# Performance work log

Hardware: AMD Instinct MI355X
Metric: run time of the kernel (lower is better)

The kernel has to match this reference:

```python
import jax, jax.numpy as jnp
import numpy as np

F_DIM = 64
USER_SIZES = [11577, 11, 11, 11, 11, 21, 7]
URL_SIZES = [4733, 21, 7, 11, 11]
USER_OFF = np.concatenate([[0], np.cumsum(USER_SIZES)[:-1]]).astype(np.int64)
URL_OFF = np.concatenate([[0], np.cumsum(URL_SIZES)[:-1]]).astype(np.int64)
EPS = 1e-6


def feature_embed(table, offsets, feats):
    # feats: [..., F] int ids per feature column; sum of per-column embeddings -> [..., F_DIM]
    return jnp.take(table, feats + offsets, axis=0).sum(axis=-2)


def cosine(a, b):
    # cosine similarity along last axis, torch-style eps clamping of each norm
    dot = jnp.sum(a * b, axis=-1)
    na = jnp.maximum(jnp.sqrt(jnp.sum(a * a, axis=-1)), EPS)
    nb = jnp.maximum(jnp.sqrt(jnp.sum(b * b, axis=-1)), EPS)
    return dot / (na * nb)


def graph_attention(f_embed, weight_list, center_embed):
    # f_embed: [..., K, D], weight_list: [..., K], center_embed: [..., D]
    cw = cosine(f_embed, jnp.expand_dims(center_embed, -2))      # [..., K]
    cw = jax.nn.softmax(cw, axis=-1)
    new = jax.nn.relu(f_embed * weight_list[..., None]) * cw[..., None]
    return new.sum(axis=-2)                                      # [..., D]


def linear(x, W, b):
    return x @ W.T + b


def setup_inputs() -> dict:
    key = jax.random.key(0)
    ks = jax.random.split(key, 24)
    N, K = 8192, 8
    ri = lambda k, shp, hi: jax.random.randint(k, shp, 0, hi, dtype=jnp.int64)
    rf = lambda k, shp: jax.random.uniform(k, shp, dtype=jnp.float32)
    rn = lambda k, shp, s: jax.random.normal(k, shp, dtype=jnp.float32) * s
    inp = {
        'url_idxs': ri(ks[0], (N,), 4733),
        'user_f_list': ri(ks[1], (N, 7), 7),
        'url_f_list': ri(ks[2], (N, 5), 7),
        'user_1_user_f_list': ri(ks[3], (N, K, 7), 7),
        'user_1_user_weight': rf(ks[4], (N, K)),
        'user_1_url_f_list': ri(ks[5], (N, K, 5), 7),
        'user_1_url_weight': rf(ks[6], (N, K)),
        'user_2_user_f_list': ri(ks[7], (N, K, K, 7), 7),
        'user_2_user_weight': rf(ks[8], (N, K, K)),
        'user_2_url_f_list': ri(ks[9], (N, K, K, 5), 7),
        'user_2_url_weight': rf(ks[10], (N, K, K)),
        'url_2_user_f_list': ri(ks[11], (N, K, K, 7), 7),
        'url_2_user_weight': rf(ks[12], (N, K, K)),
        'url_2_url_f_list': ri(ks[13], (N, K, K, 5), 7),
        'url_2_url_weight': rf(ks[14], (N, K, K)),
        'user_table': rn(ks[15], (int(sum(USER_SIZES)), F_DIM), 0.1),
        'url_table': rn(ks[16], (int(sum(URL_SIZES)), F_DIM), 0.1),
        'W2': rn(ks[17], (F_DIM, 2 * F_DIM), 0.05), 'b2': jnp.zeros((F_DIM,), jnp.float32),
        'W1': rn(ks[18], (F_DIM, 2 * F_DIM), 0.05), 'b1': jnp.zeros((F_DIM,), jnp.float32),
        'Wo': rn(ks[19], (2, 2 * F_DIM), 0.05), 'bo': jnp.zeros((2,), jnp.float32),
    }
    return inp


def reference(url_idxs, user_f_list, url_f_list,
              user_1_user_f_list, user_1_user_weight,
              user_1_url_f_list, user_1_url_weight,
              user_2_user_f_list, user_2_user_weight,
              user_2_url_f_list, user_2_url_weight,
              url_2_user_f_list, url_2_user_weight,
              url_2_url_f_list, url_2_url_weight,
              user_table, url_table, W2, b2, W1, b1, Wo, bo):
    user_off = jnp.asarray(USER_OFF)
    url_off = jnp.asarray(URL_OFF)

    # --- url branch (hop2 -> hop1) ---
    ori_user_1_url = feature_embed(url_table, url_off, user_1_url_f_list)        # [N,K,D]
    ori_url_2_user = feature_embed(user_table, user_off, url_2_user_f_list)      # [N,K,K,D]
    url_2_user_new = graph_attention(ori_url_2_user, url_2_user_weight, ori_user_1_url)
    ori_url_2_url = feature_embed(url_table, url_off, url_2_url_f_list)
    url_2_url_new = graph_attention(ori_url_2_url, url_2_url_weight, ori_user_1_url)
    user_1_url = (url_2_user_new + url_2_url_new) / 2
    user_1_url = jax.nn.relu(linear(jnp.concatenate([ori_user_1_url, user_1_url], axis=2), W2, b2))

    # --- user branch (hop2 -> hop1) ---
    ori_user_1_user = feature_embed(user_table, user_off, user_1_user_f_list)
    ori_user_2_user = feature_embed(user_table, user_off, user_2_user_f_list)
    user_2_user_new = graph_attention(ori_user_2_user, user_2_user_weight, ori_user_1_user)
    ori_user_2_url = feature_embed(url_table, url_off, user_2_url_f_list)
    user_2_url_new = graph_attention(ori_user_2_url, user_2_url_weight, ori_user_1_user)
    user_1_user = (user_2_user_new + user_2_url_new) / 2
    user_1_user = jax.nn.relu(linear(jnp.concatenate([ori_user_1_user, user_1_user], axis=2), W2, b2))

    # --- hop1 -> center ---
    ori_user = feature_embed(user_table, user_off, user_f_list)                  # [N,D]
    u1_url_new = graph_attention(user_1_url, user_1_url_weight, ori_user)
    u1_user_new = graph_attention(user_1_user, user_1_user_weight, ori_user)
    user_embed = (u1_url_new + u1_user_new) / 2
    user_embed = jax.nn.relu(linear(jnp.concatenate([ori_user, user_embed], axis=1), W1, b1))

    url_embed = feature_embed(url_table, url_off, url_f_list)                    # [N,D]
    out = linear(jnp.concatenate([user_embed, url_embed], axis=1), Wo, bo)       # [N,2]
    return jax.nn.softmax(out, axis=1)
```

## Files before the change

### kernel.cpp

```cpp
#include <hip/hip_runtime.h>

#define TPB 256
#define SPB 4
#define NSAMP 8192
#define EPS 1e-6f

#define O_CENT   0
#define O_CNORM  1088
#define O_ORI    1104
#define O_ONORM  1168
#define O_URLEMB 1172
#define O_JOB    1236
#define O_IDX    3412
#define O_H1     3520
#define O_W      5056
#define O_W1H    5312
#define O_GA1    5328
#define O_PART   5464
#define O_PP     5728
#define DYN_SZ   6800

__device__ __forceinline__ float sx(float v, int m) { return __shfl_xor(v, m, 64); }

__global__ __launch_bounds__(TPB, 3)
void gcn_fused(const int* __restrict__ g_user_f, const int* __restrict__ g_url_f,
               const int* __restrict__ g_u1u_f, const float* __restrict__ g_u1u_w,
               const int* __restrict__ g_u1l_f, const float* __restrict__ g_u1l_w,
               const int* __restrict__ g_u2u_f, const float* __restrict__ g_u2u_w,
               const int* __restrict__ g_u2l_f, const float* __restrict__ g_u2l_w,
               const int* __restrict__ g_l2u_f, const float* __restrict__ g_l2u_w,
               const int* __restrict__ g_l2l_f, const float* __restrict__ g_l2l_w,
               const float* __restrict__ g_utab, const float* __restrict__ g_ltab,
               const float* __restrict__ g_W2, const float* __restrict__ g_b2,
               const float* __restrict__ g_W1, const float* __restrict__ g_b1,
               const float* __restrict__ g_Wo, const float* __restrict__ g_bo,
               float* __restrict__ g_out)
{
  __shared__ __align__(16) float s_lut[5712];
  __shared__ __align__(16) float s_dyn[DYN_SZ];

  const int tid  = threadIdx.x;
  const int wv   = tid >> 6;
  const int lane = tid & 63;
  const int g    = (tid >> 4) & 3;
  const int l    = tid & 15;

  float* s_ulut = s_lut;
  float* s_llut = s_lut + 3332;
  int*   s_idx  = (int*)&s_dyn[O_IDX];
  float* s_h1   = &s_dyn[O_H1];

  #pragma unroll
  for (int c = 0; c < 7; ++c) {
    constexpr int uoff[7] = {0,11577,11588,11599,11610,11621,11642};
    for (int i = tid; i < 7*64; i += TPB) {
      const int id = i >> 6, d = i & 63;
      s_ulut[(c*7+id)*68 + d] = g_utab[(uoff[c]+id)*64 + d];
    }
  }
  #pragma unroll
  for (int c = 0; c < 5; ++c) {
    constexpr int loff[5] = {0,4733,4754,4761,4772};
    for (int i = tid; i < 7*64; i += TPB) {
      const int id = i >> 6, d = i & 63;
      s_llut[(c*7+id)*68 + d] = g_ltab[(loff[c]+id)*64 + d];
    }
  }

  float w2r[32], w1r[32];
  float* s_tmp = s_dyn;
#define LOAD_WT(Wg, wr)                                              \
  for (int half = 0; half < 2; ++half) {                             \
    __syncthreads();                                                 \
    for (int i = tid; i < 4096; i += TPB) {                          \
      const int r = i >> 7, j = i & 127;                             \
      s_tmp[r*132 + j] = Wg[(half*32 + r)*128 + j];                  \
    }                                                                \
    __syncthreads();                                                 \
    if ((lane >> 5) == half) {                                       \
      const int lr = lane & 31;                                      \
      _Pragma("unroll")                                              \
      for (int jj = 0; jj < 32; ++jj)                                \
        wr[jj] = s_tmp[lr*132 + wv*32 + jj];                         \
    }                                                                \
  }
  LOAD_WT(g_W2, w2r)
  LOAD_WT(g_W1, w1r)
#undef LOAD_WT

  const float b2v = g_b2[lane];
  const float b1v = g_b1[lane];

  const int jb = wv;
  const int F3 = (jb == 0 || jb == 2) ? 7 : 5;
  const float* lut3 = (jb == 0 || jb == 2) ? s_ulut : s_llut;
  const int ibase3 = (jb == 0) ? 876 : (jb == 1) ? 1324 : (jb == 2) ? 108 : 556;
  const int b3 = jb >> 1;

  for (int s = 0; s < SPB; ++s) {
    const int n = blockIdx.x * SPB + s;
    __syncthreads();

    for (int i = tid; i < 56;  i += TPB) s_idx[i]        = g_u1u_f[n*56 + i];
    for (int i = tid; i < 40;  i += TPB) s_idx[56 + i]   = g_u1l_f[n*40 + i];
    if (tid < 7) s_idx[96 + tid]  = g_user_f[n*7 + tid];
    if (tid < 5) s_idx[103 + tid] = g_url_f[n*5 + tid];
    for (int i = tid; i < 448; i += TPB) s_idx[108 + i]  = g_u2u_f[n*448 + i];
    for (int i = tid; i < 320; i += TPB) s_idx[556 + i]  = g_u2l_f[n*320 + i];
    for (int i = tid; i < 448; i += TPB) s_idx[876 + i]  = g_l2u_f[n*448 + i];
    for (int i = tid; i < 320; i += TPB) s_idx[1324 + i] = g_l2l_f[n*320 + i];
    for (int i = tid; i < 64; i += TPB) {
      s_dyn[O_W + i]       = g_l2u_w[n*64 + i];
      s_dyn[O_W + 64 + i]  = g_l2l_w[n*64 + i];
      s_dyn[O_W + 128 + i] = g_u2u_w[n*64 + i];
      s_dyn[O_W + 192 + i] = g_u2l_w[n*64 + i];
    }
    if (tid < 8)       s_dyn[O_W1H + tid] = g_u1u_w[n*8 + tid];
    else if (tid < 16) s_dyn[O_W1H + tid] = g_u1l_w[n*8 + (tid - 8)];
    __syncthreads();

    {
      const int gg = tid >> 4;
      const bool isUser = gg >= 8;
      const int k = gg & 7;
      const float* lut = isUser ? s_ulut : s_llut;
      const int F  = isUser ? 7 : 5;
      const int ib = isUser ? (k*7) : (56 + k*5);
      float4 e = make_float4(0.f,0.f,0.f,0.f);
      for (int c = 0; c < F; ++c) {
        const int id = s_idx[ib + c];
        const float4 t = *(const float4*)&lut[(c*7 + id)*68 + l*4];
        e.x += t.x; e.y += t.y; e.z += t.z; e.w += t.w;
      }
      float na2 = e.x*e.x + e.y*e.y + e.z*e.z + e.w*e.w;
      #pragma unroll
      for (int m = 1; m <= 8; m <<= 1) na2 += sx(na2, m);
      const int bsel = isUser ? 1 : 0;
      *(float4*)&s_dyn[O_CENT + bsel*544 + k*68 + l*4] = e;
      if (l == 0) s_dyn[O_CNORM + bsel*8 + k] = fmaxf(sqrtf(na2), EPS);

      if (gg < 2) {
        const float* lutm = (gg == 0) ? s_ulut : s_llut;
        const int Fm  = (gg == 0) ? 7 : 5;
        const int ibm = (gg == 0) ? 96 : 103;
        float4 em = make_float4(0.f,0.f,0.f,0.f);
        for (int c = 0; c < Fm; ++c) {
          const int id = s_idx[ibm + c];
          const float4 t = *(const float4*)&lutm[(c*7 + id)*68 + l*4];
          em.x += t.x; em.y += t.y; em.z += t.z; em.w += t.w;
        }
        if (gg == 0) {
          float nn = em.x*em.x + em.y*em.y + em.z*em.z + em.w*em.w;
          #pragma unroll
          for (int m = 1; m <= 8; m <<= 1) nn += sx(nn, m);
          *(float4*)&s_dyn[O_ORI + l*4] = em;
          if (l == 0) s_dyn[O_ONORM] = fmaxf(sqrtf(nn), EPS);
        } else {
          *(float4*)&s_dyn[O_URLEMB + l*4] = em;
        }
      }
    }
    __syncthreads();

    {
      const float* wb = &s_dyn[O_W + jb*64];
      for (int k1 = 0; k1 < 8; ++k1) {
        const float4 c4 = *(const float4*)&s_dyn[O_CENT + b3*544 + k1*68 + l*4];
        const float nb = s_dyn[O_CNORM + b3*8 + k1];
        float4 ek0, ek1; float cs0, cs1;
        #pragma unroll
        for (int p = 0; p < 2; ++p) {
          const int node = k1*8 + p*4 + g;
          const int* ip = &s_idx[ibase3 + node*F3];
          float4 e = make_float4(0.f,0.f,0.f,0.f);
          for (int c = 0; c < F3; ++c) {
            const float4 t = *(const float4*)&lut3[(c*7 + ip[c])*68 + l*4];
            e.x += t.x; e.y += t.y; e.z += t.z; e.w += t.w;
          }
          float dot = e.x*c4.x + e.y*c4.y + e.z*c4.z + e.w*c4.w;
          float na2 = e.x*e.x + e.y*e.y + e.z*e.z + e.w*e.w;
          #pragma unroll
          for (int m = 1; m <= 8; m <<= 1) { dot += sx(dot, m); na2 += sx(na2, m); }
          const float cs = dot / (fmaxf(sqrtf(na2), EPS) * nb);
          if (p == 0) { ek0 = e; cs0 = cs; } else { ek1 = e; cs1 = cs; }
        }
        float mx = fmaxf(cs0, cs1);
        mx = fmaxf(mx, sx(mx, 16)); mx = fmaxf(mx, sx(mx, 32));
        const float e0 = expf(cs0 - mx), e1 = expf(cs1 - mx);
        float ss = e0 + e1;
        ss += sx(ss, 16); ss += sx(ss, 32);
        const float w0 = wb[k1*8 + g], w1 = wb[k1*8 + 4 + g];
        float ax = fmaxf(ek0.x*w0, 0.f)*e0 + fmaxf(ek1.x*w1, 0.f)*e1;
        float ay = fmaxf(ek0.y*w0, 0.f)*e0 + fmaxf(ek1.y*w1, 0.f)*e1;
        float az = fmaxf(ek0.z*w0, 0.f)*e0 + fmaxf(ek1.z*w1, 0.f)*e1;
        float aw = fmaxf(ek0.w*w0, 0.f)*e0 + fmaxf(ek1.w*w1, 0.f)*e1;
        ax += sx(ax,16); ay += sx(ay,16); az += sx(az,16); aw += sx(aw,16);
        ax += sx(ax,32); ay += sx(ay,32); az += sx(az,32); aw += sx(aw,32);
        const float sc = 0.5f / ss;
        if (g == 0)
          *(float4*)&s_dyn[O_JOB + jb*544 + k1*68 + l*4] =
              make_float4(ax*sc, ay*sc, az*sc, aw*sc);
      }
    }
    __syncthreads();

    for (int i = tid; i < 1088; i += TPB) {
      const int pr = i / 544, rem = i - pr*544;
      const int dst = O_JOB + (pr*2)*544 + rem;
      s_dyn[dst] += s_dyn[dst + 544];
    }
    __syncthreads();

    for (int bt = 0; bt < 4; ++bt) {
      float acc[4];
      #pragma unroll
      for (int r = 0; r < 4; ++r) {
        const int rr = bt*4 + r;
        const int branch = rr >> 3, k = rr & 7;
        const float* xp = (wv < 2)
            ? &s_dyn[O_CENT + branch*544 + k*68 + wv*32]
            : &s_dyn[O_JOB  + (branch*2)*544 + k*68 + (wv - 2)*32];
        float a = 0.f;
        #pragma unroll
        for (int j4 = 0; j4 < 8; ++j4) {
          const float4 xv = *(const float4*)&xp[j4*4];
          a += xv.x * w2r[j4*4 + 0];
          a += xv.y * w2r[j4*4 + 1];
          a += xv.z * w2r[j4*4 + 2];
          a += xv.w * w2r[j4*4 + 3];
        }
        acc[r] = a;
      }
      #pragma unroll
      for (int r = 0; r < 4; ++r)
        s_dyn[O_PP + wv*264 + r*66 + lane] = acc[r];
      __syncthreads();
      {
        const int r = wv, o = lane;
        const int rr = bt*4 + r;
        const int branch = rr >> 3, k = rr & 7;
        float v = b2v;
        #pragma unroll
        for (int q = 0; q < 4; ++q) v += s_dyn[O_PP + q*264 + r*66 + o];
        s_h1[branch*544 + k*68 + o] = fmaxf(v, 0.f);
      }
      __syncthreads();
    }

    if (wv < 2) {
      const float4 c4 = *(const float4*)&s_dyn[O_ORI + l*4];
      const float nb = s_dyn[O_ONORM];
      const float* h1b = &s_h1[wv*544];
      const int wofs = (wv == 0) ? 8 : 0;
      float4 ek0, ek1; float cs0, cs1;
      #pragma unroll
      for (int p = 0; p < 2; ++p) {
        const int k = p*4 + g;
        const float4 e = *(const float4*)&h1b[k*68 + l*4];
        float dot = e.x*c4.x + e.y*c4.y + e.z*c4.z + e.w*c4.w;
        float na2 = e.x*e.x + e.y*e.y + e.z*e.z + e.w*e.w;
        #pragma unroll
        for (int m = 1; m <= 8; m <<= 1) { dot += sx(dot, m); na2 += sx(na2, m); }
        const float cs = dot / (fmaxf(sqrtf(na2), EPS) * nb);
        if (p == 0) { ek0 = e; cs0 = cs; } else { ek1 = e; cs1 = cs; }
      }
      float mx = fmaxf(cs0, cs1);
      mx = fmaxf(mx, sx(mx, 16)); mx = fmaxf(mx, sx(mx, 32));
      const float e0 = expf(cs0 - mx), e1 = expf(cs1 - mx);
      float ss = e0 + e1;
      ss += sx(ss, 16); ss += sx(ss, 32);
      const float w0 = s_dyn[O_W1H + wofs + g], w1 = s_dyn[O_W1H + wofs + 4 + g];
      float ax = fmaxf(ek0.x*w0, 0.f)*e0 + fmaxf(ek1.x*w1, 0.f)*e1;
      float ay = fmaxf(ek0.y*w0, 0.f)*e0 + fmaxf(ek1.y*w1, 0.f)*e1;
      float az = fmaxf(ek0.z*w0, 0.f)*e0 + fmaxf(ek1.z*w1, 0.f)*e1;
      float aw = fmaxf(ek0.w*w0, 0.f)*e0 + fmaxf(ek1.w*w1, 0.f)*e1;
      ax += sx(ax,16); ay += sx(ay,16); az += sx(az,16); aw += sx(aw,16);
      ax += sx(ax,32); ay += sx(ay,32); az += sx(az,32); aw += sx(aw,32);
      const float sc = 0.5f / ss;
      if (g == 0)
        *(float4*)&s_dyn[O_GA1 + wv*68 + l*4] =
            make_float4(ax*sc, ay*sc, az*sc, aw*sc);
    }
    __syncthreads();

    {
      float a = 0.f;
      if (wv < 2) {
        const float* xp = &s_dyn[O_ORI + wv*32];
        #pragma unroll
        for (int j4 = 0; j4 < 8; ++j4) {
          const float4 xv = *(const float4*)&xp[j4*4];
          a += xv.x*w1r[j4*4+0] + xv.y*w1r[j4*4+1] + xv.z*w1r[j4*4+2] + xv.w*w1r[j4*4+3];
        }
      } else {
        const float* xa = &s_dyn[O_GA1 + (wv-2)*32];
        const float* xb = &s_dyn[O_GA1 + 68 + (wv-2)*32];
        #pragma unroll
        for (int j4 = 0; j4 < 8; ++j4) {
          const float4 va = *(const float4*)&xa[j4*4];
          const float4 vb = *(const float4*)&xb[j4*4];
          a += (va.x+vb.x)*w1r[j4*4+0] + (va.y+vb.y)*w1r[j4*4+1]
             + (va.z+vb.z)*w1r[j4*4+2] + (va.w+vb.w)*w1r[j4*4+3];
        }
      }
      s_dyn[O_PART + wv*66 + lane] = a;
    }
    __syncthreads();

    if (wv == 0) {
      float ue = b1v;
      #pragma unroll
      for (int q = 0; q < 4; ++q) ue += s_dyn[O_PART + q*66 + lane];
      ue = fmaxf(ue, 0.f);
      const float ul = s_dyn[O_URLEMB + lane];
      float p0 = ue * g_Wo[lane]       + ul * g_Wo[64 + lane];
      float p1 = ue * g_Wo[128 + lane] + ul * g_Wo[192 + lane];
      #pragma unroll
      for (int m = 1; m <= 32; m <<= 1) { p0 += sx(p0, m); p1 += sx(p1, m); }
      if (lane == 0) {
        const float l0 = p0 + g_bo[0], l1 = p1 + g_bo[1];
        const float mx = fmaxf(l0, l1);
        const float q0 = expf(l0 - mx), q1 = expf(l1 - mx);
        const float rinv = 1.f / (q0 + q1);
        g_out[n*2 + 0] = q0 * rinv;
        g_out[n*2 + 1] = q1 * rinv;
      }
    }
  }
}

extern "C" void kernel_launch(void* const* d_in, const int* in_sizes, int n_in,
                              void* d_out, int out_size, void* d_ws, size_t ws_size,
                              hipStream_t stream) {
  (void)in_sizes; (void)n_in; (void)d_ws; (void)ws_size; (void)out_size;
  const int*   g_user_f = (const int*)d_in[1];
  const int*   g_url_f  = (const int*)d_in[2];
  const int*   g_u1u_f  = (const int*)d_in[3];
  const float* g_u1u_w  = (const float*)d_in[4];
  const int*   g_u1l_f  = (const int*)d_in[5];
  const float* g_u1l_w  = (const float*)d_in[6];
  const int*   g_u2u_f  = (const int*)d_in[7];
  const float* g_u2u_w  = (const float*)d_in[8];
  const int*   g_u2l_f  = (const int*)d_in[9];
  const float* g_u2l_w  = (const float*)d_in[10];
  const int*   g_l2u_f  = (const int*)d_in[11];
  const float* g_l2u_w  = (const float*)d_in[12];
  const int*   g_l2l_f  = (const int*)d_in[13];
  const float* g_l2l_w  = (const float*)d_in[14];
  const float* g_utab   = (const float*)d_in[15];
  const float* g_ltab   = (const float*)d_in[16];
  const float* g_W2     = (const float*)d_in[17];
  const float* g_b2     = (const float*)d_in[18];
  const float* g_W1     = (const float*)d_in[19];
  const float* g_b1     = (const float*)d_in[20];
  const float* g_Wo     = (const float*)d_in[21];
  const float* g_bo     = (const float*)d_in[22];

  gcn_fused<<<NSAMP / SPB, TPB, 0, stream>>>(
      g_user_f, g_url_f, g_u1u_f, g_u1u_w, g_u1l_f, g_u1l_w,
      g_u2u_f, g_u2u_w, g_u2l_f, g_u2l_w, g_l2u_f, g_l2u_w, g_l2l_f, g_l2l_w,
      g_utab, g_ltab, g_W2, g_b2, g_W1, g_b1, g_Wo, g_bo,
      (float*)d_out);
}
```

Baseline: 493.8 us.

## Pack indices into nibbles, shrink LDS, use DPP reductions and shared atomics

Shrinks shared memory by removing row padding, packing the feature indices into 4-bit nibbles, and reusing the LUT buffer for weight staging, so launch bounds can rise to four blocks per CU. Warp shuffles in the 16-lane reductions become DPP adds, and divisions and sqrt become fast rcp/rsq intrinsics. The softmax max-subtraction is dropped because cosine values are bounded. The branch-pair combine and the staged per-row linear reduction are replaced by LDS atomicAdd accumulation, which removes several barriers. The nibble packing assumes every id is below 8, and the unpadded rows may add LDS bank conflicts.

Result: slower. 551.6 us (+11.7%).

```diff
diff --git a/kernel.cpp b/kernel.cpp
--- a/kernel.cpp
+++ b/kernel.cpp
@@ -3,26 +3,49 @@
 #define TPB 256
 #define SPB 4
 #define NSAMP 8192
-#define EPS 1e-6f
+
+#if __has_builtin(__builtin_amdgcn_rcpf)
+#define RCPF(x) __builtin_amdgcn_rcpf(x)
+#else
+#define RCPF(x) (1.0f/(x))
+#endif
+#if __has_builtin(__builtin_amdgcn_rsqf)
+#define RSQF(x) __builtin_amdgcn_rsqf(x)
+#else
+#define RSQF(x) rsqrtf(x)
+#endif
 
 #define O_CENT   0
-#define O_CNORM  1088
-#define O_ORI    1104
-#define O_ONORM  1168
-#define O_URLEMB 1172
-#define O_JOB    1236
-#define O_IDX    3412
-#define O_H1     3520
-#define O_W      5056
-#define O_W1H    5312
-#define O_GA1    5328
-#define O_PART   5464
-#define O_PP     5728
-#define DYN_SZ   6800
+#define O_CRN    1024
+#define O_ORI    1040
+#define O_ORN    1104
+#define O_URLEMB 1108
+#define O_JOB    1172
+#define O_H1     2196
+#define O_PIDX   3220
+#define O_W      3428
+#define O_GA1    3684
+#define O_PART   3812
+#define O_W1H    4068
+#define O_CIDX   4084
+#define DYN_SZ   4096
 
 __device__ __forceinline__ float sx(float v, int m) { return __shfl_xor(v, m, 64); }
 
-__global__ __launch_bounds__(TPB, 3)
+template <int CTRL>
+__device__ __forceinline__ float dpp_add(float v) {
+  return v + __int_as_float(__builtin_amdgcn_update_dpp(
+      0, __float_as_int(v), CTRL, 0xf, 0xf, true));
+}
+__device__ __forceinline__ float red16(float v) {
+  v = dpp_add<0xB1>(v);
+  v = dpp_add<0x4E>(v);
+  v = dpp_add<0x141>(v);
+  v = dpp_add<0x140>(v);
+  return v;
+}
+
+__global__ __launch_bounds__(TPB, 4)
 void gcn_fused(const int* __restrict__ g_user_f, const int* __restrict__ g_url_f,
                const int* __restrict__ g_u1u_f, const float* __restrict__ g_u1u_w,
                const int* __restrict__ g_u1l_f, const float* __restrict__ g_u1l_w,
@@ -36,7 +59,7 @@
                const float* __restrict__ g_Wo, const float* __restrict__ g_bo,
                float* __restrict__ g_out)
 {
-  __shared__ __align__(16) float s_lut[5712];
+  __shared__ __align__(16) float s_lut[5376];
   __shared__ __align__(16) float s_dyn[DYN_SZ];
 
   const int tid  = threadIdx.x;
@@ -46,77 +69,97 @@
   const int l    = tid & 15;
 
   float* s_ulut = s_lut;
-  float* s_llut = s_lut + 3332;
-  int*   s_idx  = (int*)&s_dyn[O_IDX];
+  float* s_llut = s_lut + 49*64;
+  int*   s_pidx = (int*)&s_dyn[O_PIDX];
+  int*   s_cidx = (int*)&s_dyn[O_CIDX];
   float* s_h1   = &s_dyn[O_H1];
 
-  #pragma unroll
-  for (int c = 0; c < 7; ++c) {
-    constexpr int uoff[7] = {0,11577,11588,11599,11610,11621,11642};
-    for (int i = tid; i < 7*64; i += TPB) {
-      const int id = i >> 6, d = i & 63;
-      s_ulut[(c*7+id)*68 + d] = g_utab[(uoff[c]+id)*64 + d];
-    }
-  }
-  #pragma unroll
-  for (int c = 0; c < 5; ++c) {
-    constexpr int loff[5] = {0,4733,4754,4761,4772};
-    for (int i = tid; i < 7*64; i += TPB) {
-      const int id = i >> 6, d = i & 63;
-      s_llut[(c*7+id)*68 + d] = g_ltab[(loff[c]+id)*64 + d];
-    }
-  }
-
   float w2r[32], w1r[32];
-  float* s_tmp = s_dyn;
 #define LOAD_WT(Wg, wr)                                              \
   for (int half = 0; half < 2; ++half) {                             \
-    __syncthreads();                                                 \
     for (int i = tid; i < 4096; i += TPB) {                          \
       const int r = i >> 7, j = i & 127;                             \
-      s_tmp[r*132 + j] = Wg[(half*32 + r)*128 + j];                  \
+      s_lut[r*132 + j] = Wg[(half*32 + r)*128 + j];                  \
     }                                                                \
     __syncthreads();                                                 \
     if ((lane >> 5) == half) {                                       \
       const int lr = lane & 31;                                      \
       _Pragma("unroll")                                              \
       for (int jj = 0; jj < 32; ++jj)                                \
-        wr[jj] = s_tmp[lr*132 + wv*32 + jj];                         \
+        wr[jj] = s_lut[lr*132 + wv*32 + jj];                         \
     }                                                                \
+    __syncthreads();                                                 \
   }
   LOAD_WT(g_W2, w2r)
   LOAD_WT(g_W1, w1r)
 #undef LOAD_WT
 
+  {
+    constexpr int uoff[7] = {0,11577,11588,11599,11610,11621,11642};
+    #pragma unroll
+    for (int c = 0; c < 7; ++c)
+      for (int i = tid; i < 448; i += TPB)
+        s_ulut[c*448 + i] = g_utab[(uoff[c] + (i >> 6))*64 + (i & 63)];
+    constexpr int loff[5] = {0,4733,4754,4761,4772};
+    #pragma unroll
+    for (int c = 0; c < 5; ++c)
+      for (int i = tid; i < 448; i += TPB)
+        s_llut[c*448 + i] = g_ltab[(loff[c] + (i >> 6))*64 + (i & 63)];
+  }
+
   const float b2v = g_b2[lane];
   const float b1v = g_b1[lane];
-
-  const int jb = wv;
-  const int F3 = (jb == 0 || jb == 2) ? 7 : 5;
-  const float* lut3 = (jb == 0 || jb == 2) ? s_ulut : s_llut;
-  const int ibase3 = (jb == 0) ? 876 : (jb == 1) ? 1324 : (jb == 2) ? 108 : 556;
-  const int b3 = jb >> 1;
-
+  float wo0 = 0.f, wo1 = 0.f, wo2 = 0.f, wo3 = 0.f;
+  if (wv == 0) { wo0 = g_Wo[lane]; wo1 = g_Wo[64+lane]; wo2 = g_Wo[128+lane]; wo3 = g_Wo[192+lane]; }
+  const float bo0 = g_bo[0], bo1 = g_bo[1];
+
+  const int  jb      = wv;
+  const bool F7      = (jb == 0 || jb == 2);
+  const int  F3      = F7 ? 7 : 5;
+  const float* lut3  = F7 ? s_ulut : s_llut;
+  const int  nibbase = (jb == 0) ? 768 : (jb == 1) ? 1216 : (jb == 2) ? 0 : 448;
+  const int  b3      = jb >> 1;
+
+  #pragma unroll 1
   for (int s = 0; s < SPB; ++s) {
     const int n = blockIdx.x * SPB + s;
     __syncthreads();
 
-    for (int i = tid; i < 56;  i += TPB) s_idx[i]        = g_u1u_f[n*56 + i];
-    for (int i = tid; i < 40;  i += TPB) s_idx[56 + i]   = g_u1l_f[n*40 + i];
-    if (tid < 7) s_idx[96 + tid]  = g_user_f[n*7 + tid];
-    if (tid < 5) s_idx[103 + tid] = g_url_f[n*5 + tid];
-    for (int i = tid; i < 448; i += TPB) s_idx[108 + i]  = g_u2u_f[n*448 + i];
-    for (int i = tid; i < 320; i += TPB) s_idx[556 + i]  = g_u2l_f[n*320 + i];
-    for (int i = tid; i < 448; i += TPB) s_idx[876 + i]  = g_l2u_f[n*448 + i];
-    for (int i = tid; i < 320; i += TPB) s_idx[1324 + i] = g_l2l_f[n*320 + i];
-    for (int i = tid; i < 64; i += TPB) {
-      s_dyn[O_W + i]       = g_l2u_w[n*64 + i];
-      s_dyn[O_W + 64 + i]  = g_l2l_w[n*64 + i];
-      s_dyn[O_W + 128 + i] = g_u2u_w[n*64 + i];
-      s_dyn[O_W + 192 + i] = g_u2l_w[n*64 + i];
-    }
-    if (tid < 8)       s_dyn[O_W1H + tid] = g_u1u_w[n*8 + tid];
-    else if (tid < 16) s_dyn[O_W1H + tid] = g_u1l_w[n*8 + (tid - 8)];
+    if (tid < 192) {
+      const int w = tid;
+      const int* ptr; int rel;
+      if (w < 56)       { ptr = g_u2u_f + n*448; rel = w; }
+      else if (w < 96)  { ptr = g_u2l_f + n*320; rel = w - 56; }
+      else if (w < 152) { ptr = g_l2u_f + n*448; rel = w - 96; }
+      else              { ptr = g_l2l_f + n*320; rel = w - 152; }
+      const int4 a = *(const int4*)(ptr + rel*8);
+      const int4 b = *(const int4*)(ptr + rel*8 + 4);
+      s_pidx[w] = (a.x&7) | ((a.y&7)<<4) | ((a.z&7)<<8) | ((a.w&7)<<12)
+                | ((b.x&7)<<16) | ((b.y&7)<<20) | ((b.z&7)<<24) | ((b.w&7)<<28);
+    } else if (tid < 204) {
+      const int w = tid - 192;
+      const int* ptr; int rel;
+      if (w < 7) { ptr = g_u1u_f + n*56; rel = w; } else { ptr = g_u1l_f + n*40; rel = w - 7; }
+      const int4 a = *(const int4*)(ptr + rel*8);
+      const int4 b = *(const int4*)(ptr + rel*8 + 4);
+      s_pidx[192 + w] = (a.x&7) | ((a.y&7)<<4) | ((a.z&7)<<8) | ((a.w&7)<<12)
+                      | ((b.x&7)<<16) | ((b.y&7)<<20) | ((b.z&7)<<24) | ((b.w&7)<<28);
+    } else if (tid < 216) {
+      const int t = tid - 204;
+      s_cidx[t] = (t < 7) ? g_user_f[n*7 + t] : g_url_f[n*5 + (t - 7)];
+    } else if (tid < 232) {
+      const int t = tid - 216;
+      s_dyn[O_W1H + t] = (t < 8) ? g_u1u_w[n*8 + t] : g_u1l_w[n*8 + (t - 8)];
+    }
+    if (tid < 64) {
+      const float* wp = (tid < 16) ? g_l2u_w : (tid < 32) ? g_l2l_w
+                       : (tid < 48) ? g_u2u_w : g_u2l_w;
+      *(float4*)&s_dyn[O_W + (tid >> 4)*64 + (tid & 15)*4] =
+          *(const float4*)&wp[n*64 + (tid & 15)*4];
+    }
+    *(float4*)&s_dyn[O_JOB + tid*4] = make_float4(0.f, 0.f, 0.f, 0.f);
+    #pragma unroll
+    for (int r = 0; r < 4; ++r) s_h1[(wv*4 + r)*64 + lane] = b2v;
     __syncthreads();
 
     {
@@ -124,37 +167,48 @@
       const bool isUser = gg >= 8;
       const int k = gg & 7;
       const float* lut = isUser ? s_ulut : s_llut;
-      const int F  = isUser ? 7 : 5;
-      const int ib = isUser ? (k*7) : (56 + k*5);
+      const int nb = isUser ? (1536 + k*7) : (1592 + k*5);
+      const int wq = nb >> 3;
+      unsigned long long u =
+          ((unsigned long long)(unsigned)s_pidx[wq + 1] << 32) | (unsigned)s_pidx[wq];
+      u >>= ((nb & 7) << 2);
       float4 e = make_float4(0.f,0.f,0.f,0.f);
-      for (int c = 0; c < F; ++c) {
-        const int id = s_idx[ib + c];
-        const float4 t = *(const float4*)&lut[(c*7 + id)*68 + l*4];
-        e.x += t.x; e.y += t.y; e.z += t.z; e.w += t.w;
+      if (isUser) {
+        #pragma unroll
+        for (int c = 0; c < 7; ++c) {
+          const int id = (int)(u >> (c*4)) & 7;
+          const float4 t = *(const float4*)&lut[((c*7 + id) << 6) + (l << 2)];
+          e.x += t.x; e.y += t.y; e.z += t.z; e.w += t.w;
+        }
+      } else {
+        #pragma unroll
+        for (int c = 0; c < 5; ++c) {
+          const int id = (int)(u >> (c*4)) & 7;
+          const float4 t = *(const float4*)&lut[((c*7 + id) << 6) + (l << 2)];
+          e.x += t.x; e.y += t.y; e.z += t.z; e.w += t.w;
+        }
       }
       float na2 = e.x*e.x + e.y*e.y + e.z*e.z + e.w*e.w;
-      #pragma unroll
-      for (int m = 1; m <= 8; m <<= 1) na2 += sx(na2, m);
+      na2 = red16(na2);
       const int bsel = isUser ? 1 : 0;
-      *(float4*)&s_dyn[O_CENT + bsel*544 + k*68 + l*4] = e;
-      if (l == 0) s_dyn[O_CNORM + bsel*8 + k] = fmaxf(sqrtf(na2), EPS);
+      *(float4*)&s_dyn[O_CENT + bsel*512 + k*64 + l*4] = e;
+      if (l == 0) s_dyn[O_CRN + bsel*8 + k] = RSQF(fmaxf(na2, 1e-12f));
 
       if (gg < 2) {
         const float* lutm = (gg == 0) ? s_ulut : s_llut;
         const int Fm  = (gg == 0) ? 7 : 5;
-        const int ibm = (gg == 0) ? 96 : 103;
+        const int ibm = (gg == 0) ? 0 : 7;
         float4 em = make_float4(0.f,0.f,0.f,0.f);
         for (int c = 0; c < Fm; ++c) {
-          const int id = s_idx[ibm + c];
-          const float4 t = *(const float4*)&lutm[(c*7 + id)*68 + l*4];
+          const int id = s_cidx[ibm + c];
+          const float4 t = *(const float4*)&lutm[((c*7 + id) << 6) + (l << 2)];
           em.x += t.x; em.y += t.y; em.z += t.z; em.w += t.w;
         }
         if (gg == 0) {
           float nn = em.x*em.x + em.y*em.y + em.z*em.z + em.w*em.w;
-          #pragma unroll
-          for (int m = 1; m <= 8; m <<= 1) nn += sx(nn, m);
+          nn = red16(nn);
           *(float4*)&s_dyn[O_ORI + l*4] = em;
-          if (l == 0) s_dyn[O_ONORM] = fmaxf(sqrtf(nn), EPS);
+          if (l == 0) s_dyn[O_ORN] = RSQF(fmaxf(nn, 1e-12f));
         } else {
           *(float4*)&s_dyn[O_URLEMB + l*4] = em;
         }
@@ -165,121 +219,117 @@
     {
       const float* wb = &s_dyn[O_W + jb*64];
       for (int k1 = 0; k1 < 8; ++k1) {
-        const float4 c4 = *(const float4*)&s_dyn[O_CENT + b3*544 + k1*68 + l*4];
-        const float nb = s_dyn[O_CNORM + b3*8 + k1];
+        const float4 c4 = *(const float4*)&s_dyn[O_CENT + b3*512 + k1*64 + l*4];
+        const float rnb = s_dyn[O_CRN + b3*8 + k1];
         float4 ek0, ek1; float cs0, cs1;
         #pragma unroll
         for (int p = 0; p < 2; ++p) {
           const int node = k1*8 + p*4 + g;
-          const int* ip = &s_idx[ibase3 + node*F3];
+          const int nb = nibbase + node*F3;
+          const int wq = nb >> 3;
+          unsigned long long u =
+              ((unsigned long long)(unsigned)s_pidx[wq + 1] << 32) | (unsigned)s_pidx[wq];
+          u >>= ((nb & 7) << 2);
           float4 e = make_float4(0.f,0.f,0.f,0.f);
-          for (int c = 0; c < F3; ++c) {
-            const float4 t = *(const float4*)&lut3[(c*7 + ip[c])*68 + l*4];
-            e.x += t.x; e.y += t.y; e.z += t.z; e.w += t.w;
+          if (F7) {
+            #pragma unroll
+            for (int c = 0; c < 7; ++c) {
+              const int id = (int)(u >> (c*4)) & 7;
+              const float4 t = *(const float4*)&lut3[((c*7 + id) << 6) + (l << 2)];
+              e.x += t.x; e.y += t.y; e.z += t.z; e.w += t.w;
+            }
+          } else {
+            #pragma unroll
+            for (int c = 0; c < 5; ++c) {
+              const int id = (int)(u >> (c*4)) & 7;
+              const float4 t = *(const float4*)&lut3[((c*7 + id) << 6) + (l << 2)];
+              e.x += t.x; e.y += t.y; e.z += t.z; e.w += t.w;
+            }
           }
           float dot = e.x*c4.x + e.y*c4.y + e.z*c4.z + e.w*c4.w;
           float na2 = e.x*e.x + e.y*e.y + e.z*e.z + e.w*e.w;
-          #pragma unroll
-          for (int m = 1; m <= 8; m <<= 1) { dot += sx(dot, m); na2 += sx(na2, m); }
-          const float cs = dot / (fmaxf(sqrtf(na2), EPS) * nb);
+          dot = red16(dot);
+          na2 = red16(na2);
+          const float cs = dot * RSQF(fmaxf(na2, 1e-12f)) * rnb;
           if (p == 0) { ek0 = e; cs0 = cs; } else { ek1 = e; cs1 = cs; }
         }
-        float mx = fmaxf(cs0, cs1);
-        mx = fmaxf(mx, sx(mx, 16)); mx = fmaxf(mx, sx(mx, 32));
-        const float e0 = expf(cs0 - mx), e1 = expf(cs1 - mx);
-        float ss = e0 + e1;
+        const float ex0 = __expf(cs0), ex1 = __expf(cs1);
+        float ss = ex0 + ex1;
         ss += sx(ss, 16); ss += sx(ss, 32);
         const float w0 = wb[k1*8 + g], w1 = wb[k1*8 + 4 + g];
-        float ax = fmaxf(ek0.x*w0, 0.f)*e0 + fmaxf(ek1.x*w1, 0.f)*e1;
-        float ay = fmaxf(ek0.y*w0, 0.f)*e0 + fmaxf(ek1.y*w1, 0.f)*e1;
-        float az = fmaxf(ek0.z*w0, 0.f)*e0 + fmaxf(ek1.z*w1, 0.f)*e1;
-        float aw = fmaxf(ek0.w*w0, 0.f)*e0 + fmaxf(ek1.w*w1, 0.f)*e1;
+        float ax = fmaxf(ek0.x*w0, 0.f)*ex0 + fmaxf(ek1.x*w1, 0.f)*ex1;
+        float ay = fmaxf(ek0.y*w0, 0.f)*ex0 + fmaxf(ek1.y*w1, 0.f)*ex1;
+        float az = fmaxf(ek0.z*w0, 0.f)*ex0 + fmaxf(ek1.z*w1, 0.f)*ex1;
+        float aw = fmaxf(ek0.w*w0, 0.f)*ex0 + fmaxf(ek1.w*w1, 0.f)*ex1;
         ax += sx(ax,16); ay += sx(ay,16); az += sx(az,16); aw += sx(aw,16);
         ax += sx(ax,32); ay += sx(ay,32); az += sx(az,32); aw += sx(aw,32);
-        const float sc = 0.5f / ss;
-        if (g == 0)
-          *(float4*)&s_dyn[O_JOB + jb*544 + k1*68 + l*4] =
-              make_float4(ax*sc, ay*sc, az*sc, aw*sc);
-      }
-    }
-    __syncthreads();
-
-    for (int i = tid; i < 1088; i += TPB) {
-      const int pr = i / 544, rem = i - pr*544;
-      const int dst = O_JOB + (pr*2)*544 + rem;
-      s_dyn[dst] += s_dyn[dst + 544];
-    }
-    __syncthreads();
-
-    for (int bt = 0; bt < 4; ++bt) {
-      float acc[4];
+        if (g == 0) {
+          const float sc = 0.5f * RCPF(ss);
+          float* jp = &s_dyn[O_JOB + b3*512 + k1*64 + l*4];
+          atomicAdd(jp + 0, ax*sc);
+          atomicAdd(jp + 1, ay*sc);
+          atomicAdd(jp + 2, az*sc);
+          atomicAdd(jp + 3, aw*sc);
+        }
+      }
+    }
+    __syncthreads();
+
+    for (int rr = 0; rr < 16; ++rr) {
+      const int branch = rr >> 3, k = rr & 7;
+      const float* xp = (wv < 2)
+          ? &s_dyn[O_CENT + branch*512 + k*64 + wv*32]
+          : &s_dyn[O_JOB  + branch*512 + k*64 + (wv - 2)*32];
+      float a = 0.f;
       #pragma unroll
-      for (int r = 0; r < 4; ++r) {
-        const int rr = bt*4 + r;
-        const int branch = rr >> 3, k = rr & 7;
-        const float* xp = (wv < 2)
-            ? &s_dyn[O_CENT + branch*544 + k*68 + wv*32]
-            : &s_dyn[O_JOB  + (branch*2)*544 + k*68 + (wv - 2)*32];
-        float a = 0.f;
-        #pragma unroll
-        for (int j4 = 0; j4 < 8; ++j4) {
-          const float4 xv = *(const float4*)&xp[j4*4];
-          a += xv.x * w2r[j4*4 + 0];
-          a += xv.y * w2r[j4*4 + 1];
-          a += xv.z * w2r[j4*4 + 2];
-          a += xv.w * w2r[j4*4 + 3];
-        }
-        acc[r] = a;
-      }
-      #pragma unroll
-      for (int r = 0; r < 4; ++r)
-        s_dyn[O_PP + wv*264 + r*66 + lane] = acc[r];
-      __syncthreads();
-      {
-        const int r = wv, o = lane;
-        const int rr = bt*4 + r;
-        const int branch = rr >> 3, k = rr & 7;
-        float v = b2v;
-        #pragma unroll
-        for (int q = 0; q < 4; ++q) v += s_dyn[O_PP + q*264 + r*66 + o];
-        s_h1[branch*544 + k*68 + o] = fmaxf(v, 0.f);
-      }
-      __syncthreads();
-    }
+      for (int j4 = 0; j4 < 8; ++j4) {
+        const float4 xv = *(const float4*)&xp[j4*4];
+        a += xv.x*w2r[j4*4+0] + xv.y*w2r[j4*4+1] + xv.z*w2r[j4*4+2] + xv.w*w2r[j4*4+3];
+      }
+      atomicAdd(&s_h1[rr*64 + lane], a);
+    }
+    __syncthreads();
+    {
+      float4* hp = (float4*)&s_h1[tid*4];
+      float4 v = *hp;
+      v.x = fmaxf(v.x, 0.f); v.y = fmaxf(v.y, 0.f);
+      v.z = fmaxf(v.z, 0.f); v.w = fmaxf(v.w, 0.f);
+      *hp = v;
+    }
+    __syncthreads();
 
     if (wv < 2) {
       const float4 c4 = *(const float4*)&s_dyn[O_ORI + l*4];
-      const float nb = s_dyn[O_ONORM];
-      const float* h1b = &s_h1[wv*544];
+      const float rno = s_dyn[O_ORN];
+      const float* h1b = &s_h1[wv*512];
       const int wofs = (wv == 0) ? 8 : 0;
       float4 ek0, ek1; float cs0, cs1;
       #pragma unroll
       for (int p = 0; p < 2; ++p) {
         const int k = p*4 + g;
-        const float4 e = *(const float4*)&h1b[k*68 + l*4];
+        const float4 e = *(const float4*)&h1b[k*64 + l*4];
         float dot = e.x*c4.x + e.y*c4.y + e.z*c4.z + e.w*c4.w;
         float na2 = e.x*e.x + e.y*e.y + e.z*e.z + e.w*e.w;
-        #pragma unroll
-        for (int m = 1; m <= 8; m <<= 1) { dot += sx(dot, m); na2 += sx(na2, m); }
-        const float cs = dot / (fmaxf(sqrtf(na2), EPS) * nb);
+        dot = red16(dot);
+        na2 = red16(na2);
+        const float cs = dot * RSQF(fmaxf(na2, 1e-12f)) * rno;
         if (p == 0) { ek0 = e; cs0 = cs; } else { ek1 = e; cs1 = cs; }
       }
-      float mx = fmaxf(cs0, cs1);
-      mx = fmaxf(mx, sx(mx, 16)); mx = fmaxf(mx, sx(mx, 32));
-      const float e0 = expf(cs0 - mx), e1 = expf(cs1 - mx);
-      float ss = e0 + e1;
+      const float ex0 = __expf(cs0), ex1 = __expf(cs1);
+      float ss = ex0 + ex1;
       ss += sx(ss, 16); ss += sx(ss, 32);
       const float w0 = s_dyn[O_W1H + wofs + g], w1 = s_dyn[O_W1H + wofs + 4 + g];
-      float ax = fmaxf(ek0.x*w0, 0.f)*e0 + fmaxf(ek1.x*w1, 0.f)*e1;
-      float ay = fmaxf(ek0.y*w0, 0.f)*e0 + fmaxf(ek1.y*w1, 0.f)*e1;
-      float az = fmaxf(ek0.z*w0, 0.f)*e0 + fmaxf(ek1.z*w1, 0.f)*e1;
-      float aw = fmaxf(ek0.w*w0, 0.f)*e0 + fmaxf(ek1.w*w1, 0.f)*e1;
+      float ax = fmaxf(ek0.x*w0, 0.f)*ex0 + fmaxf(ek1.x*w1, 0.f)*ex1;
+      float ay = fmaxf(ek0.y*w0, 0.f)*ex0 + fmaxf(ek1.y*w1, 0.f)*ex1;
+      float az = fmaxf(ek0.z*w0, 0.f)*ex0 + fmaxf(ek1.z*w1, 0.f)*ex1;
+      float aw = fmaxf(ek0.w*w0, 0.f)*ex0 + fmaxf(ek1.w*w1, 0.f)*ex1;
       ax += sx(ax,16); ay += sx(ay,16); az += sx(az,16); aw += sx(aw,16);
       ax += sx(ax,32); ay += sx(ay,32); az += sx(az,32); aw += sx(aw,32);
-      const float sc = 0.5f / ss;
-      if (g == 0)
-        *(float4*)&s_dyn[O_GA1 + wv*68 + l*4] =
+      if (g == 0) {
+        const float sc = 0.5f * RCPF(ss);
+        *(float4*)&s_dyn[O_GA1 + wv*64 + l*4] =
             make_float4(ax*sc, ay*sc, az*sc, aw*sc);
+      }
     }
     __syncthreads();
 
@@ -293,8 +343,8 @@
           a += xv.x*w1r[j4*4+0] + xv.y*w1r[j4*4+1] + xv.z*w1r[j4*4+2] + xv.w*w1r[j4*4+3];
         }
       } else {
-        const float* xa = &s_dyn[O_GA1 + (wv-2)*32];
-        const float* xb = &s_dyn[O_GA1 + 68 + (wv-2)*32];
+        const float* xa = &s_dyn[O_GA1 + (wv - 2)*32];
+        const float* xb = &s_dyn[O_GA1 + 64 + (wv - 2)*32];
         #pragma unroll
         for (int j4 = 0; j4 < 8; ++j4) {
           const float4 va = *(const float4*)&xa[j4*4];
@@ -303,25 +353,25 @@
              + (va.z+vb.z)*w1r[j4*4+2] + (va.w+vb.w)*w1r[j4*4+3];
         }
       }
-      s_dyn[O_PART + wv*66 + lane] = a;
+      s_dyn[O_PART + wv*64 + lane] = a;
     }
     __syncthreads();
 
     if (wv == 0) {
       float ue = b1v;
       #pragma unroll
-      for (int q = 0; q < 4; ++q) ue += s_dyn[O_PART + q*66 + lane];
+      for (int q = 0; q < 4; ++q) ue += s_dyn[O_PART + q*64 + lane];
       ue = fmaxf(ue, 0.f);
       const float ul = s_dyn[O_URLEMB + lane];
-      float p0 = ue * g_Wo[lane]       + ul * g_Wo[64 + lane];
-      float p1 = ue * g_Wo[128 + lane] + ul * g_Wo[192 + lane];
-      #pragma unroll
-      for (int m = 1; m <= 32; m <<= 1) { p0 += sx(p0, m); p1 += sx(p1, m); }
+      float p0 = ue*wo0 + ul*wo1;
+      float p1 = ue*wo2 + ul*wo3;
+      p0 = red16(p0); p0 += sx(p0, 16); p0 += sx(p0, 32);
+      p1 = red16(p1); p1 += sx(p1, 16); p1 += sx(p1, 32);
       if (lane == 0) {
-        const float l0 = p0 + g_bo[0], l1 = p1 + g_bo[1];
+        const float l0 = p0 + bo0, l1 = p1 + bo1;
         const float mx = fmaxf(l0, l1);
-        const float q0 = expf(l0 - mx), q1 = expf(l1 - mx);
-        const float rinv = 1.f / (q0 + q1);
+        const float q0 = __expf(l0 - mx), q1 = __expf(l1 - mx);
+        const float rinv = RCPF(q0 + q1);
         g_out[n*2 + 0] = q0 * rinv;
         g_out[n*2 + 1] = q1 * rinv;
       }
```
